# Optimization experiments

Measured on AMD Instinct MI355X. Metric: run time of the kernel, lower is better.

Reference implementation:

```python
import jax, jax.numpy as jnp
import numpy as np

B, S, H, NH, T = 4, 512, 512, 8, 3
DH = H // NH
DTS = H // T  # 170, per-timescale encoder width
EPS = 1e-5

def _ln(x, g, b):
    m = jnp.mean(x, axis=-1, keepdims=True)
    v = jnp.mean((x - m) ** 2, axis=-1, keepdims=True)
    return (x - m) * jax.lax.rsqrt(v + EPS) * g + b

def _gelu(x):
    return jax.nn.gelu(x, approximate=False)

def _mha(x, qkv_W, qkv_b, out_W, out_b, mask):
    # x: [B,S,H]; qkv_W: [H,3H]; mask: [B,S,S] float additive or None
    qkv = x @ qkv_W + qkv_b
    q, k, v = jnp.split(qkv, 3, axis=-1)
    q = q.reshape(B, S, NH, DH)
    k = k.reshape(B, S, NH, DH)
    v = v.reshape(B, S, NH, DH)
    scores = jnp.einsum('bqhd,bkhd->bhqk', q, k) / jnp.sqrt(jnp.float32(DH))
    if mask is not None:
        scores = scores + mask[:, None, :, :]
    attn = jax.nn.softmax(scores, axis=-1)
    o = jnp.einsum('bhqk,bkhd->bqhd', attn, v).reshape(B, S, H)
    return o @ out_W + out_b

def setup_inputs() -> dict:
    key = jax.random.key(0)
    ks = jax.random.split(key, 32)
    r = lambda i, shape, s=0.02: (jax.random.normal(ks[i], shape, dtype=jnp.float32) * s)
    inp = {}
    inp['x'] = jax.random.normal(ks[0], (B, S, H), dtype=jnp.float32)
    inp['timestamps'] = jax.random.uniform(ks[1], (B, S), dtype=jnp.float32) * 1e6
    # per-timescale encoders (stacked over T)
    inp['enc_W'] = r(2, (T, 2, DTS), 0.5)
    inp['enc_b'] = jnp.zeros((T, DTS), jnp.float32)
    inp['enc_ln_g'] = jnp.ones((T, DTS), jnp.float32)
    inp['enc_ln_b'] = jnp.zeros((T, DTS), jnp.float32)
    # per-timescale MHA
    inp['qkv_W'] = r(3, (T, H, 3 * H))
    inp['qkv_b'] = jnp.zeros((T, 3 * H), jnp.float32)
    inp['attn_out_W'] = r(4, (T, H, H))
    inp['attn_out_b'] = jnp.zeros((T, H), jnp.float32)
    # time mixer
    inp['mixer_W1'] = r(5, (T * H, H))
    inp['mixer_b1'] = jnp.zeros((H,), jnp.float32)
    inp['mixer_ln_g'] = jnp.ones((H,), jnp.float32)
    inp['mixer_ln_b'] = jnp.zeros((H,), jnp.float32)
    inp['mixer_W2'] = r(6, (H, T))
    inp['mixer_b2'] = jnp.zeros((T,), jnp.float32)
    # transformer encoder layer (post-norm, gelu, ffn=4H)
    inp['el_qkv_W'] = r(7, (H, 3 * H))
    inp['el_qkv_b'] = jnp.zeros((3 * H,), jnp.float32)
    inp['el_out_W'] = r(8, (H, H))
    inp['el_out_b'] = jnp.zeros((H,), jnp.float32)
    inp['el_ln1_g'] = jnp.ones((H,), jnp.float32)
    inp['el_ln1_b'] = jnp.zeros((H,), jnp.float32)
    inp['el_ff_W1'] = r(9, (H, 4 * H))
    inp['el_ff_b1'] = jnp.zeros((4 * H,), jnp.float32)
    inp['el_ff_W2'] = r(10, (4 * H, H))
    inp['el_ff_b2'] = jnp.zeros((H,), jnp.float32)
    inp['el_ln2_g'] = jnp.ones((H,), jnp.float32)
    inp['el_ln2_b'] = jnp.zeros((H,), jnp.float32)
    # output projection
    inp['op_W'] = r(11, (H, H))
    inp['op_b'] = jnp.zeros((H,), jnp.float32)
    inp['op_ln_g'] = jnp.ones((H,), jnp.float32)
    inp['op_ln_b'] = jnp.zeros((H,), jnp.float32)
    return inp

def reference(x, timestamps, enc_W, enc_b, enc_ln_g, enc_ln_b, qkv_W, qkv_b, attn_out_W, attn_out_b,
              mixer_W1, mixer_b1, mixer_ln_g, mixer_ln_b, mixer_W2, mixer_b2,
              el_qkv_W, el_qkv_b, el_out_W, el_out_b, el_ln1_g, el_ln1_b,
              el_ff_W1, el_ff_b1, el_ff_W2, el_ff_b2, el_ln2_g, el_ln2_b,
              op_W, op_b, op_ln_g, op_ln_b):
    # pairwise time features [B,S,S]
    time_diff = timestamps[:, :, None] - timestamps[:, None, :]
    direction = jnp.sign(time_diff)
    magnitude = jnp.log1p(jnp.abs(time_diff) / 3600.0)
    outs = []
    for i in range(T):
        mag = magnitude / (10.0 ** i)
        tf = jnp.stack([direction, mag], axis=-1)            # [B,S,S,2]
        e = tf @ enc_W[i] + enc_b[i]                          # [B,S,S,DTS]
        e = _gelu(_ln(e, enc_ln_g[i], enc_ln_b[i]))
        mask = jnp.mean(e, axis=-1)                           # [B,S,S] additive attn mask
        outs.append(_mha(x, qkv_W[i], qkv_b[i], attn_out_W[i], attn_out_b[i], mask))
    combined = jnp.concatenate(outs, axis=-1)                 # [B,S,T*H]
    m = _gelu(_ln(combined @ mixer_W1 + mixer_b1, mixer_ln_g, mixer_ln_b))
    mix = jax.nn.softmax(m @ mixer_W2 + mixer_b2, axis=-1)    # [B,S,T]
    weighted = sum(mix[..., i:i + 1] * outs[i] for i in range(T))
    # post-norm transformer encoder layer
    sa = _mha(weighted, el_qkv_W, el_qkv_b, el_out_W, el_out_b, None)
    h1 = _ln(weighted + sa, el_ln1_g, el_ln1_b)
    ff = _gelu(h1 @ el_ff_W1 + el_ff_b1) @ el_ff_W2 + el_ff_b2
    h2 = _ln(h1 + ff, el_ln2_g, el_ln2_b)
    out = _ln(h2 @ op_W + op_b, op_ln_g, op_ln_b)
    return out
```

## Files before the change

### kernel.cpp

```cpp
#include <hip/hip_runtime.h>
#include <hip/hip_bf16.h>
#include <math.h>

#define Bq 4
#define Sq 512
#define Hq 512
#define NHq 8
#define Tq 3
#define DTSq 170
#define BSq 2048
#define NLUT 2048
#define MAGMAXf 5.6304994f

typedef float f32x4 __attribute__((ext_vector_type(4)));
typedef __bf16 bf16x4 __attribute__((ext_vector_type(4)));
typedef __bf16 bf16x8 __attribute__((ext_vector_type(8)));

__device__ __forceinline__ float gelu_f(float x){
  return 0.5f * x * (1.0f + erff(x * 0.70710678118654752f));
}

__device__ __forceinline__ void gload16(const void* g, void* l){
  __builtin_amdgcn_global_load_lds((const __attribute__((address_space(1))) void*)g,
                                   (__attribute__((address_space(3))) void*)l, 16, 0, 0);
}

__device__ __forceinline__ float waveReduceSum(float v){
  #pragma unroll
  for (int off = 32; off > 0; off >>= 1) v += __shfl_xor(v, off);
  return v;
}

__device__ __forceinline__ float blockReduce(float v, float* red){
  int tid = threadIdx.x;
  __syncthreads();
  red[tid] = v; __syncthreads();
  for (int s = 128; s > 0; s >>= 1){
    if (tid < s) red[tid] += red[tid + s];
    __syncthreads();
  }
  return red[0];
}

struct CvtEnt { const float* W; __bf16* WT; int ldw, ldt, ntn, start; };
struct CvtArgs { CvtEnt e[12]; };

__global__ __launch_bounds__(256) void prep_all(
    const float* __restrict__ x, __bf16* __restrict__ xb,
    CvtArgs a,
    const float* __restrict__ encW, const float* __restrict__ encB,
    const float* __restrict__ g, const float* __restrict__ be,
    float* __restrict__ lut)
{
  __shared__ float T[64][65];
  __shared__ float red[256];
  __shared__ float sw0[DTSq], sw1[DTSq], sbc[DTSq], sg[DTSq], sbe[DTSq];
  __shared__ float sS[6];
  int bid = blockIdx.x, tid = threadIdx.x;

  if (bid < 1024){
    int idx = (bid * 256 + tid) * 4;
    float4 v = *(const float4*)&x[idx];
    bf16x4 r; r[0]=(__bf16)v.x; r[1]=(__bf16)v.y; r[2]=(__bf16)v.z; r[3]=(__bf16)v.w;
    *(bf16x4*)&xb[idx] = r;
    return;
  }
  if (bid < 1024 + 1792){
    int wb = bid - 1024;
    int i = 0;
    #pragma unroll
    for (int k = 1; k < 12; ++k) if (wb >= a.e[k].start) i = k;
    const float* W = a.e[i].W;
    __bf16* WT = a.e[i].WT;
    int ldw = a.e[i].ldw, ldt = a.e[i].ldt;
    int local = wb - a.e[i].start;
    int tn = local % a.e[i].ntn, tk = local / a.e[i].ntn;
    int n0 = tn * 64, k0 = tk * 64;
    #pragma unroll
    for (int q = 0; q < 16; ++q){
      int lin = q * 256 + tid;
      int r = lin >> 6, c = lin & 63;
      T[r][c] = W[(size_t)(k0 + r) * ldw + n0 + c];
    }
    __syncthreads();
    #pragma unroll
    for (int q = 0; q < 16; ++q){
      int lin = q * 256 + tid;
      int n = lin >> 6, k = lin & 63;
      WT[(size_t)(n0 + n) * ldt + k0 + k] = (__bf16)T[k][n];
    }
    return;
  }
  int local = bid - (1024 + 1792);
  int td = local >> 3, echunk = local & 7;
  int t = td / 3, dsel = td % 3;
  float d = (float)(dsel - 1);
  const float* W0 = encW + t * 2 * DTSq;
  const float* W1 = W0 + DTSq;
  const float* Bv = encB + t * DTSq;
  float w0 = (tid < DTSq) ? W0[tid] : 0.f;
  float w1 = (tid < DTSq) ? W1[tid] : 0.f;
  float bv = (tid < DTSq) ? Bv[tid] : 0.f;
  const float invD = 1.0f / (float)DTSq;
  float m0 = blockReduce(w0, red) * invD;
  float m1 = blockReduce(w1, red) * invD;
  float mb = blockReduce(bv, red) * invD;
  float c0 = (tid < DTSq) ? (w0 - m0) : 0.f;
  float c1 = (tid < DTSq) ? (w1 - m1) : 0.f;
  float cb = (tid < DTSq) ? (bv - mb) : 0.f;
  if (tid < DTSq){
    sw0[tid] = c0; sw1[tid] = c1; sbc[tid] = cb;
    sg[tid] = g[t * DTSq + tid]; sbe[tid] = be[t * DTSq + tid];
  }
  float pa = blockReduce(c0 * c0, red) * invD;
  float pb = blockReduce(c1 * c1, red) * invD;
  float pc = blockReduce(c0 * c1, red) * invD;
  float pd = blockReduce(c0 * cb, red) * invD;
  float pe = blockReduce(c1 * cb, red) * invD;
  float pf = blockReduce(cb * cb, red) * invD;
  if (tid == 0){ sS[0]=pa; sS[1]=pb; sS[2]=pc; sS[3]=pd; sS[4]=pe; sS[5]=pf; }
  __syncthreads();
  float A = sS[0], Bs = sS[1], Cs = sS[2], Ds = sS[3], Es = sS[4], Fs = sS[5];
  int e = echunk * 256 + tid;
  float tscale = (t == 0) ? 1.f : ((t == 1) ? 0.1f : 0.01f);
  float m = (MAGMAXf / (float)(NLUT - 1)) * (float)e * tscale;
  float var = fabsf(d) * A + m * m * Bs + Fs + 2.f * (d * m * Cs + d * Ds + m * Es);
  float rs = rsqrtf(var + 1e-5f);
  float sum = 0.f;
  for (int c = 0; c < DTSq; ++c){
    float ee = fmaf(m, sw1[c], fmaf(d, sw0[c], sbc[c]));
    float n = fmaf(ee * rs, sg[c], sbe[c]);
    sum += n * 0.5f * (1.0f + erff(n * 0.70710678118654752f));
  }
  lut[td * NLUT + e] = sum * (1.0f / (float)DTSq);
}

__global__ __launch_bounds__(256) void mask_fill(const float* __restrict__ ts,
                                                 const float* __restrict__ lut,
                                                 __bf16* __restrict__ maskbuf){
  int bi = blockIdx.x;
  int b = bi >> 9, i = bi & 511;
  float tsi = ts[bi];
  for (int j0 = 0; j0 < Sq; j0 += 256){
    int j = j0 + threadIdx.x;
    float dt = tsi - ts[(b << 9) + j];
    int dsel = (dt > 0.f) ? 2 : ((dt < 0.f) ? 0 : 1);
    float mag = log1pf(fabsf(dt) * (1.0f / 3600.0f));
    float u = mag * ((float)(NLUT - 1) / MAGMAXf);
    int i0 = (int)u; if (i0 > NLUT - 2) i0 = NLUT - 2;
    float f = u - (float)i0;
    #pragma unroll
    for (int t = 0; t < Tq; ++t){
      const float* lp = lut + (t * 3 + dsel) * NLUT + i0;
      float v = lp[0] + f * (lp[1] - lp[0]);
      maskbuf[(((size_t)(t * Bq + b) * Sq + i) * Sq) + j] = (__bf16)v;
    }
  }
}

template<int BM, int BN, int BK>
__global__ __launch_bounds__(256) void gemm_pipe(
    const __bf16* __restrict__ A, int lda, size_t sAz,
    const __bf16* __restrict__ BT, int ldb, size_t sBz,
    const float* __restrict__ bias, int sBiasz,
    float* __restrict__ C32, __bf16* __restrict__ C16, int ldc, size_t sCz,
    int K, int act)
{
  constexpr int MF = BM / 32;
  constexpr int NF = BN / 32;
  constexpr int ROWB = BK * 2;
  constexpr int SWZM = (BK == 64) ? 7 : 15;
  constexpr int ALOADS = BM * ROWB / 4096;
  constexpr int BLOADS = BN * ROWB / 4096;
  constexpr int LOADS = ALOADS + BLOADS;
  constexpr int ABYTES = BM * ROWB;
  constexpr int BBYTES = BN * ROWB;
  __shared__ __bf16 lds[(2 * (ABYTES + BBYTES)) / 2];
  int tid = threadIdx.x;

  int gx = gridDim.x, nwg = gx * gridDim.y;
  int lin = blockIdx.x + gx * blockIdx.y;
  int q8 = nwg >> 3;
  int swz = (lin & 7) * q8 + (lin >> 3);
  int bx = swz % gx, by = swz / gx;

  int z = blockIdx.z;
  A  += (size_t)z * sAz;
  BT += (size_t)z * sBz;
  const float* bz = bias ? bias + (size_t)z * sBiasz : nullptr;
  size_t cbase = (size_t)z * sCz;
  int brow = by * BM, bcol = bx * BN;

  int lane = tid & 63, w = tid >> 6;
  int wr = (w >> 1) * (BM / 2), wc = (w & 1) * (BN / 2);
  int lr = lane & 15, lg = lane >> 4;

  f32x4 acc[MF][NF];
  #pragma unroll
  for (int m = 0; m < MF; ++m)
    #pragma unroll
    for (int n = 0; n < NF; ++n) acc[m][n] = (f32x4){0.f, 0.f, 0.f, 0.f};

  char* lbase = (char*)lds;

  auto stage = [&](int buf, int ko){
    char* ab = lbase + buf * (ABYTES + BBYTES);
    #pragma unroll
    for (int qq = 0; qq < ALOADS; ++qq){
      int byte = (qq * 256 + tid) * 16;
      int row = byte / ROWB, col = byte % ROWB;
      int src = col ^ ((row & SWZM) << 4);
      gload16(&A[(size_t)(brow + row) * lda + ko + (src >> 1)], ab + byte);
    }
    char* bb = ab + ABYTES;
    #pragma unroll
    for (int qq = 0; qq < BLOADS; ++qq){
      int byte = (qq * 256 + tid) * 16;
      int row = byte / ROWB, col = byte % ROWB;
      int src = col ^ ((row & SWZM) << 4);
      gload16(&BT[(size_t)(bcol + row) * ldb + ko + (src >> 1)], bb + byte);
    }
  };

  stage(0, 0);
  int nk = K / BK;
  for (int kt = 0; kt < nk; ++kt){
    int cur = kt & 1;
    if (kt + 1 < nk){
      stage(cur ^ 1, (kt + 1) * BK);
      if constexpr (LOADS == 3)      asm volatile("s_waitcnt vmcnt(3)" ::: "memory");
      else if constexpr (LOADS == 4) asm volatile("s_waitcnt vmcnt(4)" ::: "memory");
      else                           asm volatile("s_waitcnt vmcnt(6)" ::: "memory");
    } else {
      asm volatile("s_waitcnt vmcnt(0)" ::: "memory");
    }
    __builtin_amdgcn_s_barrier();
    __builtin_amdgcn_sched_barrier(0);
    char* ab = lbase + cur * (ABYTES + BBYTES);
    char* bb = ab + ABYTES;
    #pragma unroll
    for (int s = 0; s < BK / 32; ++s){
      bf16x8 af[MF], bfr[NF];
      #pragma unroll
      for (int m = 0; m < MF; ++m){
        int row = wr + m * 16 + lr;
        int col = (s * 64 + lg * 16) ^ ((row & SWZM) << 4);
        af[m] = *(const bf16x8*)(ab + row * ROWB + col);
      }
      #pragma unroll
      for (int n = 0; n < NF; ++n){
        int row = wc + n * 16 + lr;
        int col = (s * 64 + lg * 16) ^ ((row & SWZM) << 4);
        bfr[n] = *(const bf16x8*)(bb + row * ROWB + col);
      }
      #pragma unroll
      for (int m = 0; m < MF; ++m)
        #pragma unroll
        for (int n = 0; n < NF; ++n)
          acc[m][n] = __builtin_amdgcn_mfma_f32_16x16x32_bf16(af[m], bfr[n], acc[m][n], 0, 0, 0);
    }
    asm volatile("" ::: "memory");
    __builtin_amdgcn_s_barrier();
  }

  #pragma unroll
  for (int m = 0; m < MF; ++m){
    #pragma unroll
    for (int n = 0; n < NF; ++n){
      int col = bcol + wc + n * 16 + lr;
      float bv = bz ? bz[col] : 0.f;
      #pragma unroll
      for (int j = 0; j < 4; ++j){
        int row = brow + wr + m * 16 + lg * 4 + j;
        float v = acc[m][n][j] + bv;
        if (act) v = gelu_f(v);
        size_t idx = cbase + (size_t)row * ldc + col;
        if (C32) C32[idx] = v;
        if (C16) C16[idx] = (__bf16)v;
      }
    }
  }
}

template<bool HM>
__global__ __launch_bounds__(256) void flash_attn(
    const __bf16* __restrict__ qkv, size_t sQz,
    const __bf16* __restrict__ vt,  size_t sVz,
    const __bf16* __restrict__ mask, size_t sMz,
    __bf16* __restrict__ ctx, size_t sCz)
{
  int t = blockIdx.z;
  qkv += (size_t)t * sQz;
  vt  += (size_t)t * sVz;
  ctx += (size_t)t * sCz;
  const __bf16* mk = HM ? mask + (size_t)t * sMz : nullptr;

  int lin = blockIdx.x + (blockIdx.y << 3);
  int swz = (lin & 7) * 32 + (lin >> 3);
  int io = (swz & 7) * 64;
  int bh = swz >> 3;
  int b = bh >> 3, h = bh & 7;

  constexpr int TB = 8192;
  constexpr int BUFB = HM ? 3 * TB : 2 * TB;
  __shared__ char lds[2 * BUFB + (HM ? 0 : TB)];
  char* lb = lds;
  int tid = threadIdx.x, lane = tid & 63, w = tid >> 6;
  int lr = lane & 15, lg = lane >> 4;

  const __bf16* qrow = &qkv[(size_t)(b * Sq + io + w * 16 + lr) * 1536 + h * 64];
  bf16x8 q0 = *(const bf16x8*)&qrow[lg * 8];
  bf16x8 q1 = *(const bf16x8*)&qrow[32 + lg * 8];

  auto stage = [&](int buf, int jo){
    char* kb = lb + buf * BUFB;
    #pragma unroll
    for (int qq = 0; qq < 2; ++qq){
      int byte = (qq * 256 + tid) * 16;
      int row = byte >> 7;
      int src = (byte & 127) ^ ((row & 7) << 4);
      gload16(&qkv[(size_t)(b * Sq + jo + row) * 1536 + 512 + h * 64 + (src >> 1)], kb + byte);
    }
    char* vb = kb + TB;
    #pragma unroll
    for (int qq = 0; qq < 2; ++qq){
      int byte = (qq * 256 + tid) * 16;
      int row = byte >> 7;
      int src = (byte & 127) ^ ((row & 7) << 4);
      gload16(&vt[((size_t)bh * 64 + row) * Sq + jo + (src >> 1)], vb + byte);
    }
    if constexpr (HM){
      char* mb = vb + TB;
      #pragma unroll
      for (int qq = 0; qq < 2; ++qq){
        int byte = (qq * 256 + tid) * 16;
        int row = byte >> 7;
        int src = (byte & 127) ^ ((row & 7) << 4);
        gload16(&mk[(size_t)(b * Sq + io + row) * Sq + jo + (src >> 1)], mb + byte);
      }
    }
  };

  f32x4 o[4];
  #pragma unroll
  for (int n = 0; n < 4; ++n) o[n] = (f32x4){0.f, 0.f, 0.f, 0.f};
  float mrow[4] = {-1e30f, -1e30f, -1e30f, -1e30f};
  float lrow[4] = {0.f, 0.f, 0.f, 0.f};

  stage(0, 0);
  #pragma unroll
  for (int kt = 0; kt < 8; ++kt){
    int cur = kt & 1;

    if (kt + 1 < 8){
      stage(cur ^ 1, (kt + 1) << 6);
      if constexpr (HM) asm volatile("s_waitcnt vmcnt(6)" ::: "memory");
      else              asm volatile("s_waitcnt vmcnt(4)" ::: "memory");
    } else {
      asm volatile("s_waitcnt vmcnt(0)" ::: "memory");
    }
    __builtin_amdgcn_s_barrier();
    __builtin_amdgcn_sched_barrier(0);

    char* kb = lb + cur * BUFB;
    char* vb = kb + TB;
    char* mb = HM ? vb + TB : lb + 2 * BUFB;

    f32x4 s4[4];
    #pragma unroll
    for (int n = 0; n < 4; ++n) s4[n] = (f32x4){0.f, 0.f, 0.f, 0.f};
    __builtin_amdgcn_s_setprio(1);
    #pragma unroll
    for (int s = 0; s < 2; ++s){
      bf16x8 aq = s ? q1 : q0;
      #pragma unroll
      for (int n = 0; n < 4; ++n){
        int row = n * 16 + lr;
        int colb = (s * 64 + lg * 16) ^ ((row & 7) << 4);
        bf16x8 bk = *(const bf16x8*)(kb + row * 128 + colb);
        s4[n] = __builtin_amdgcn_mfma_f32_16x16x32_bf16(aq, bk, s4[n], 0, 0, 0);
      }
    }
    __builtin_amdgcn_s_setprio(0);

    float sv[4][4];
    #pragma unroll
    for (int n = 0; n < 4; ++n){
      #pragma unroll
      for (int reg = 0; reg < 4; ++reg){
        float v = s4[n][reg] * 0.125f;
        if constexpr (HM){
          int row = w * 16 + lg * 4 + reg;
          int off = ((n * 16 + lr) * 2) ^ ((row & 7) << 4);
          v += (float)*(const __bf16*)(mb + row * 128 + off);
        }
        sv[n][reg] = v;
      }
    }

    #pragma unroll
    for (int reg = 0; reg < 4; ++reg){
      float pmax = fmaxf(fmaxf(sv[0][reg], sv[1][reg]), fmaxf(sv[2][reg], sv[3][reg]));
      #pragma unroll
      for (int off = 1; off < 16; off <<= 1) pmax = fmaxf(pmax, __shfl_xor(pmax, off));
      if (pmax > mrow[reg] + 8.0f){
        float corr = __expf(mrow[reg] - pmax);
        mrow[reg] = pmax;
        lrow[reg] *= corr;
        #pragma unroll
        for (int n = 0; n < 4; ++n) o[n][reg] *= corr;
      }
      float rs = 0.f;
      #pragma unroll
      for (int n = 0; n < 4; ++n){
        float p = __expf(sv[n][reg] - mrow[reg]);
        sv[n][reg] = p;
        rs += p;
      }
      #pragma unroll
      for (int off = 1; off < 16; off <<= 1) rs += __shfl_xor(rs, off);
      lrow[reg] += rs;
    }

    #pragma unroll
    for (int n = 0; n < 4; ++n)
      #pragma unroll
      for (int reg = 0; reg < 4; ++reg){
        int row = w * 16 + lg * 4 + reg;
        int off = ((n * 16 + lr) * 2) ^ ((row & 7) << 4);
        *(__bf16*)(mb + row * 128 + off) = (__bf16)sv[n][reg];
      }
    __builtin_amdgcn_s_setprio(1);
    #pragma unroll
    for (int s = 0; s < 2; ++s){
      int arow = w * 16 + lr;
      int acol = (s * 64 + lg * 16) ^ ((arow & 7) << 4);
      bf16x8 ap = *(const bf16x8*)(mb + arow * 128 + acol);
      #pragma unroll
      for (int n = 0; n < 4; ++n){
        int row = n * 16 + lr;
        int colb = (s * 64 + lg * 16) ^ ((row & 7) << 4);
        bf16x8 bv = *(const bf16x8*)(vb + row * 128 + colb);
        o[n] = __builtin_amdgcn_mfma_f32_16x16x32_bf16(ap, bv, o[n], 0, 0, 0);
      }
    }
    __builtin_amdgcn_s_setprio(0);

    asm volatile("" ::: "memory");
    __builtin_amdgcn_s_barrier();
  }

  #pragma unroll
  for (int reg = 0; reg < 4; ++reg){
    float inv = 1.0f / lrow[reg];
    int row = b * Sq + io + w * 16 + lg * 4 + reg;
    #pragma unroll
    for (int n = 0; n < 4; ++n)
      ctx[(size_t)row * Hq + h * 64 + n * 16 + lr] = (__bf16)(o[n][reg] * inv);
  }
}

__global__ __launch_bounds__(256) void ln_rows(const float* __restrict__ in,
                                               const float* __restrict__ res,
                                               const float* __restrict__ g,
                                               const float* __restrict__ bb,
                                               float* __restrict__ out32,
                                               __bf16* __restrict__ out16,
                                               int do_gelu){
  int row = blockIdx.x * 4 + (threadIdx.x >> 6);
  int lane = threadIdx.x & 63;
  const float* ir = in + (size_t)row * Hq;
  const float* rr = res ? res + (size_t)row * Hq : nullptr;
  float x[8]; float s = 0.f, sq = 0.f;
  #pragma unroll
  for (int k = 0; k < 8; ++k){
    int c = lane + 64 * k;
    float v = ir[c];
    if (rr) v += rr[c];
    x[k] = v; s += v; sq += v * v;
  }
  s = waveReduceSum(s); sq = waveReduceSum(sq);
  float mean = s * (1.0f / Hq);
  float var = fmaxf(sq * (1.0f / Hq) - mean * mean, 0.f);
  float rstd = rsqrtf(var + 1e-5f);
  #pragma unroll
  for (int k = 0; k < 8; ++k){
    int c = lane + 64 * k;
    float y = (x[k] - mean) * rstd * g[c] + bb[c];
    if (do_gelu) y = gelu_f(y);
    if (out32) out32[(size_t)row * Hq + c] = y;
    if (out16) out16[(size_t)row * Hq + c] = (__bf16)y;
  }
}

__global__ __launch_bounds__(256) void ln_mixer_weighted(const float* __restrict__ in,
                                                         const float* __restrict__ g,
                                                         const float* __restrict__ bb,
                                                         const float* __restrict__ W2,
                                                         const float* __restrict__ b2,
                                                         const __bf16* __restrict__ comb,
                                                         float* __restrict__ out32,
                                                         __bf16* __restrict__ out16){
  int row = blockIdx.x * 4 + (threadIdx.x >> 6);
  int lane = threadIdx.x & 63;
  const float* ir = in + (size_t)row * Hq;
  float x[8]; float s = 0.f, sq = 0.f;
  #pragma unroll
  for (int k = 0; k < 8; ++k){
    int c = lane + 64 * k;
    float v = ir[c];
    x[k] = v; s += v; sq += v * v;
  }
  s = waveReduceSum(s); sq = waveReduceSum(sq);
  float mean = s * (1.0f / Hq);
  float var = fmaxf(sq * (1.0f / Hq) - mean * mean, 0.f);
  float rstd = rsqrtf(var + 1e-5f);
  float a0 = 0.f, a1 = 0.f, a2 = 0.f;
  #pragma unroll
  for (int k = 0; k < 8; ++k){
    int c = lane + 64 * k;
    float y = gelu_f((x[k] - mean) * rstd * g[c] + bb[c]);
    const float* wv = W2 + c * 3;
    a0 = fmaf(y, wv[0], a0); a1 = fmaf(y, wv[1], a1); a2 = fmaf(y, wv[2], a2);
  }
  a0 = waveReduceSum(a0) + b2[0];
  a1 = waveReduceSum(a1) + b2[1];
  a2 = waveReduceSum(a2) + b2[2];
  float mx = fmaxf(a0, fmaxf(a1, a2));
  float e0 = __expf(a0 - mx), e1 = __expf(a1 - mx), e2 = __expf(a2 - mx);
  float inv = 1.0f / (e0 + e1 + e2);
  float m0 = e0 * inv, m1 = e1 * inv, m2 = e2 * inv;
  const __bf16* cr = comb + (size_t)row * 1536;
  #pragma unroll
  for (int k = 0; k < 8; ++k){
    int c = lane + 64 * k;
    float v = m0 * (float)cr[c] + m1 * (float)cr[512 + c] + m2 * (float)cr[1024 + c];
    out32[(size_t)row * Hq + c] = v;
    out16[(size_t)row * Hq + c] = (__bf16)v;
  }
}

__global__ __launch_bounds__(256) void transpose_v(const __bf16* __restrict__ qkv, size_t sQz,
                                                   __bf16* __restrict__ vt, size_t sVz){
  int t = blockIdx.z;
  qkv += (size_t)t * sQz;
  vt  += (size_t)t * sVz;
  int bh = blockIdx.y, b = bh >> 3, h = bh & 7;
  int so = blockIdx.x * 64;
  __shared__ __bf16 T[64][72];
  int tid = threadIdx.x;
  #pragma unroll
  for (int q = 0; q < 16; ++q){
    int lin = q * 256 + tid;
    int r = lin >> 6, c = lin & 63;
    T[r][c] = qkv[(size_t)(b * Sq + so + r) * 1536 + 1024 + h * 64 + c];
  }
  __syncthreads();
  #pragma unroll
  for (int q = 0; q < 16; ++q){
    int lin = q * 256 + tid;
    int d = lin >> 6, s = lin & 63;
    vt[((size_t)bh * 64 + d) * Sq + so + s] = T[s][d];
  }
}

extern "C" void kernel_launch(void* const* d_in, const int* in_sizes, int n_in,
                              void* d_out, int out_size, void* d_ws, size_t ws_size,
                              hipStream_t stream){
  const float* x         = (const float*)d_in[0];
  const float* ts        = (const float*)d_in[1];
  const float* enc_W     = (const float*)d_in[2];
  const float* enc_b     = (const float*)d_in[3];
  const float* enc_ln_g  = (const float*)d_in[4];
  const float* enc_ln_b  = (const float*)d_in[5];
  const float* qkv_W     = (const float*)d_in[6];
  const float* qkv_b     = (const float*)d_in[7];
  const float* aout_W    = (const float*)d_in[8];
  const float* aout_b    = (const float*)d_in[9];
  const float* mx_W1     = (const float*)d_in[10];
  const float* mx_b1     = (const float*)d_in[11];
  const float* mx_ln_g   = (const float*)d_in[12];
  const float* mx_ln_b   = (const float*)d_in[13];
  const float* mx_W2     = (const float*)d_in[14];
  const float* mx_b2     = (const float*)d_in[15];
  const float* el_qkv_W  = (const float*)d_in[16];
  const float* el_qkv_b  = (const float*)d_in[17];
  const float* el_out_W  = (const float*)d_in[18];
  const float* el_out_b  = (const float*)d_in[19];
  const float* el_ln1_g  = (const float*)d_in[20];
  const float* el_ln1_b  = (const float*)d_in[21];
  const float* el_ff_W1  = (const float*)d_in[22];
  const float* el_ff_b1  = (const float*)d_in[23];
  const float* el_ff_W2  = (const float*)d_in[24];
  const float* el_ff_b2  = (const float*)d_in[25];
  const float* el_ln2_g  = (const float*)d_in[26];
  const float* el_ln2_b  = (const float*)d_in[27];
  const float* op_W      = (const float*)d_in[28];
  const float* op_b      = (const float*)d_in[29];
  const float* op_ln_g   = (const float*)d_in[30];
  const float* op_ln_b   = (const float*)d_in[31];

  float* ws = (float*)d_ws;
  size_t o = 0;
  __bf16* MASKBb = (__bf16*)(ws + o); o += 1572864;
  __bf16* XB     = (__bf16*)(ws + o); o += 524288;
  __bf16* qkvT   = (__bf16*)(ws + o); o += 1179648;
  __bf16* aoutT  = (__bf16*)(ws + o); o += 393216;
  __bf16* mx1T   = (__bf16*)(ws + o); o += 393216;
  __bf16* elqkvT = (__bf16*)(ws + o); o += 393216;
  __bf16* eloutT = (__bf16*)(ws + o); o += 131072;
  __bf16* ff1T   = (__bf16*)(ws + o); o += 524288;
  __bf16* ff2T   = (__bf16*)(ws + o); o += 524288;
  __bf16* opT    = (__bf16*)(ws + o); o += 131072;
  __bf16* QKVb   = (__bf16*)(ws + o); o += 4718592;
  __bf16* VTb    = (__bf16*)(ws + o); o += 1572864;
  __bf16* FFBb   = (__bf16*)(ws + o); o += 2097152;
  __bf16* CTXb   = (__bf16*)(ws + o); o += 1572864;
  __bf16* COMBb  = (__bf16*)(ws + o); o += 1572864;
  float*  MBUF   = ws + o;            o += 1048576;
  float*  WEI    = ws + o;            o += 1048576;
  __bf16* WEIb   = (__bf16*)(ws + o); o += 524288;
  float*  SA     = ws + o;            o += 1048576;
  float*  H1     = ws + o;            o += 1048576;
  __bf16* H1b    = (__bf16*)(ws + o); o += 524288;
  float*  H2     = ws + o;            o += 1048576;
  __bf16* H2b    = (__bf16*)(ws + o); o += 524288;
  float*  LUTB   = ws + o;            o += 9 * NLUT;
  float*  OPO    = MBUF;

  {
    CvtArgs ca;
    for (int t = 0; t < 3; ++t)
      ca.e[t] = {qkv_W + (size_t)t * 512 * 1536, qkvT + (size_t)t * 1536 * 512, 1536, 512, 24, 192 * t};
    for (int t = 0; t < 3; ++t)
      ca.e[3 + t] = {aout_W + (size_t)t * 512 * 512, aoutT + (size_t)t * 512 * 512, 512, 512, 8, 576 + 64 * t};
    ca.e[6]  = {mx_W1,    mx1T,   512,  1536, 8,  768};
    ca.e[7]  = {el_qkv_W, elqkvT, 1536, 512,  24, 960};
    ca.e[8]  = {el_out_W, eloutT, 512,  512,  8,  1152};
    ca.e[9]  = {el_ff_W1, ff1T,   2048, 512,  32, 1216};
    ca.e[10] = {el_ff_W2, ff2T,   512,  2048, 8,  1472};
    ca.e[11] = {op_W,     opT,    512,  512,  8,  1728};
    prep_all<<<1024 + 1792 + 72, 256, 0, stream>>>(x, XB, ca, enc_W, enc_b,
                                                   enc_ln_g, enc_ln_b, LUTB);
  }
  mask_fill<<<BSq, 256, 0, stream>>>(ts, LUTB, MASKBb);

  gemm_pipe<128,64,64><<<dim3(24, 16, 3), 256, 0, stream>>>(XB, 512, 0, qkvT, 512, (size_t)1536 * 512,
      qkv_b, 1536, nullptr, QKVb, 1536, (size_t)2048 * 1536, 512, 0);
  transpose_v<<<dim3(8, 32, 3), 256, 0, stream>>>(QKVb, (size_t)2048 * 1536, VTb, (size_t)32 * 64 * 512);
  flash_attn<true><<<dim3(8, 32, 3), 256, 0, stream>>>(QKVb, (size_t)2048 * 1536,
      VTb, (size_t)32 * 64 * 512, MASKBb, (size_t)4 * 512 * 512, CTXb, (size_t)2048 * 512);
  gemm_pipe<64,32,128><<<dim3(16, 32, 3), 256, 0, stream>>>(CTXb, 512, (size_t)2048 * 512, aoutT, 512, (size_t)512 * 512,
      aout_b, 512, nullptr, COMBb, 1536, 512, 512, 0);

  gemm_pipe<64,32,128><<<dim3(16, 32, 1), 256, 0, stream>>>(COMBb, 1536, 0, mx1T, 1536, 0,
      mx_b1, 0, MBUF, nullptr, 512, 0, 1536, 0);
  ln_mixer_weighted<<<512, 256, 0, stream>>>(MBUF, mx_ln_g, mx_ln_b, mx_W2, mx_b2, COMBb, WEI, WEIb);

  gemm_pipe<128,64,64><<<dim3(24, 16, 1), 256, 0, stream>>>(WEIb, 512, 0, elqkvT, 512, 0,
      el_qkv_b, 0, nullptr, QKVb, 1536, 0, 512, 0);
  transpose_v<<<dim3(8, 32, 1), 256, 0, stream>>>(QKVb, 0, VTb, 0);
  flash_attn<false><<<dim3(8, 32, 1), 256, 0, stream>>>(QKVb, 0, VTb, 0, nullptr, 0, CTXb, 0);
  gemm_pipe<64,32,128><<<dim3(16, 32, 1), 256, 0, stream>>>(CTXb, 512, 0, eloutT, 512, 0,
      el_out_b, 0, SA, nullptr, 512, 0, 512, 0);
  ln_rows<<<512, 256, 0, stream>>>(WEI, SA, el_ln1_g, el_ln1_b, H1, H1b, 0);
  gemm_pipe<128,64,64><<<dim3(32, 16, 1), 256, 0, stream>>>(H1b, 512, 0, ff1T, 512, 0,
      el_ff_b1, 0, nullptr, FFBb, 2048, 0, 512, 1);
  gemm_pipe<64,32,128><<<dim3(16, 32, 1), 256, 0, stream>>>(FFBb, 2048, 0, ff2T, 2048, 0,
      el_ff_b2, 0, SA, nullptr, 512, 0, 2048, 0);
  ln_rows<<<512, 256, 0, stream>>>(H1, SA, el_ln2_g, el_ln2_b, H2, H2b, 0);

  gemm_pipe<64,32,128><<<dim3(16, 32, 1), 256, 0, stream>>>(H2b, 512, 0, opT, 512, 0,
      op_b, 0, OPO, nullptr, 512, 0, 512, 0);
  ln_rows<<<512, 256, 0, stream>>>(OPO, nullptr, op_ln_g, op_ln_b, (float*)d_out, nullptr, 0);
}
```

Before: 208.7 us.

## Compute timestamp mask inside flash attention from LDS-resident LUT

Removes the mask_fill kernel and the bf16 [3,B,S,S] mask buffer. The masked flash attention now loads timestamps and a smaller per-timescale LUT into LDS and computes the additive mask per score element (log1p plus interpolation). The LUT shrinks from 2048 to 512 entries so it fits in LDS, which cuts LUT prep blocks but coarsens interpolation accuracy. This trades mask memory traffic and a kernel launch for extra ALU work per score inside attention.

```diff
diff --git a/kernel.cpp b/kernel.cpp
--- a/kernel.cpp
+++ b/kernel.cpp
@@ -9,7 +9,7 @@
 #define Tq 3
 #define DTSq 170
 #define BSq 2048
-#define NLUT 2048
+#define NLUT 512
 #define MAGMAXf 5.6304994f
 
 typedef float f32x4 __attribute__((ext_vector_type(4)));
@@ -92,7 +92,7 @@
     return;
   }
   int local = bid - (1024 + 1792);
-  int td = local >> 3, echunk = local & 7;
+  int td = local >> 1, echunk = local & 1;
   int t = td / 3, dsel = td % 3;
   float d = (float)(dsel - 1);
   const float* W0 = encW + t * 2 * DTSq;
@@ -135,29 +135,6 @@
   lut[td * NLUT + e] = sum * (1.0f / (float)DTSq);
 }
 
-__global__ __launch_bounds__(256) void mask_fill(const float* __restrict__ ts,
-                                                 const float* __restrict__ lut,
-                                                 __bf16* __restrict__ maskbuf){
-  int bi = blockIdx.x;
-  int b = bi >> 9, i = bi & 511;
-  float tsi = ts[bi];
-  for (int j0 = 0; j0 < Sq; j0 += 256){
-    int j = j0 + threadIdx.x;
-    float dt = tsi - ts[(b << 9) + j];
-    int dsel = (dt > 0.f) ? 2 : ((dt < 0.f) ? 0 : 1);
-    float mag = log1pf(fabsf(dt) * (1.0f / 3600.0f));
-    float u = mag * ((float)(NLUT - 1) / MAGMAXf);
-    int i0 = (int)u; if (i0 > NLUT - 2) i0 = NLUT - 2;
-    float f = u - (float)i0;
-    #pragma unroll
-    for (int t = 0; t < Tq; ++t){
-      const float* lp = lut + (t * 3 + dsel) * NLUT + i0;
-      float v = lp[0] + f * (lp[1] - lp[0]);
-      maskbuf[(((size_t)(t * Bq + b) * Sq + i) * Sq) + j] = (__bf16)v;
-    }
-  }
-}
-
 template<int BM, int BN, int BK>
 __global__ __launch_bounds__(256) void gemm_pipe(
     const __bf16* __restrict__ A, int lda, size_t sAz,
@@ -286,14 +263,14 @@
 __global__ __launch_bounds__(256) void flash_attn(
     const __bf16* __restrict__ qkv, size_t sQz,
     const __bf16* __restrict__ vt,  size_t sVz,
-    const __bf16* __restrict__ mask, size_t sMz,
+    const float* __restrict__ tsg,
+    const float* __restrict__ lutg,
     __bf16* __restrict__ ctx, size_t sCz)
 {
   int t = blockIdx.z;
   qkv += (size_t)t * sQz;
   vt  += (size_t)t * sVz;
   ctx += (size_t)t * sCz;
-  const __bf16* mk = HM ? mask + (size_t)t * sMz : nullptr;
 
   int lin = blockIdx.x + (blockIdx.y << 3);
   int swz = (lin & 7) * 32 + (lin >> 3);
@@ -302,15 +279,29 @@
   int b = bh >> 3, h = bh & 7;
 
   constexpr int TB = 8192;
-  constexpr int BUFB = HM ? 3 * TB : 2 * TB;
-  __shared__ char lds[2 * BUFB + (HM ? 0 : TB)];
+  constexpr int BUFB = 2 * TB;
+  __shared__ char lds[2 * BUFB + TB + (HM ? 8192 : 0)];
   char* lb = lds;
+  char* psb = lb + 2 * BUFB;
+  float* tsL  = (float*)(lb + 2 * BUFB + TB);
+  float* lutL = (float*)(lb + 2 * BUFB + TB + 2048);
   int tid = threadIdx.x, lane = tid & 63, w = tid >> 6;
   int lr = lane & 15, lg = lane >> 4;
 
   const __bf16* qrow = &qkv[(size_t)(b * Sq + io + w * 16 + lr) * 1536 + h * 64];
   bf16x8 q0 = *(const bf16x8*)&qrow[lg * 8];
   bf16x8 q1 = *(const bf16x8*)&qrow[32 + lg * 8];
+
+  if constexpr (HM){
+    const float* tsrow = tsg + b * Sq;
+    const float* lrow  = lutg + t * 3 * NLUT;
+    #pragma unroll
+    for (int qq = 0; qq < 2; ++qq){
+      int c = qq * 256 + tid;
+      if (c < 128) gload16(tsrow + c * 4, (char*)tsL + c * 16);
+      else         gload16(lrow + (c - 128) * 4, (char*)lutL + (c - 128) * 16);
+    }
+  }
 
   auto stage = [&](int buf, int jo){
     char* kb = lb + buf * BUFB;
@@ -329,16 +320,6 @@
       int src = (byte & 127) ^ ((row & 7) << 4);
       gload16(&vt[((size_t)bh * 64 + row) * Sq + jo + (src >> 1)], vb + byte);
     }
-    if constexpr (HM){
-      char* mb = vb + TB;
-      #pragma unroll
-      for (int qq = 0; qq < 2; ++qq){
-        int byte = (qq * 256 + tid) * 16;
-        int row = byte >> 7;
-        int src = (byte & 127) ^ ((row & 7) << 4);
-        gload16(&mk[(size_t)(b * Sq + io + row) * Sq + jo + (src >> 1)], mb + byte);
-      }
-    }
   };
 
   f32x4 o[4];
@@ -351,11 +332,11 @@
   #pragma unroll
   for (int kt = 0; kt < 8; ++kt){
     int cur = kt & 1;
+    int jo = kt << 6;
 
     if (kt + 1 < 8){
       stage(cur ^ 1, (kt + 1) << 6);
-      if constexpr (HM) asm volatile("s_waitcnt vmcnt(6)" ::: "memory");
-      else              asm volatile("s_waitcnt vmcnt(4)" ::: "memory");
+      asm volatile("s_waitcnt vmcnt(4)" ::: "memory");
     } else {
       asm volatile("s_waitcnt vmcnt(0)" ::: "memory");
     }
@@ -364,7 +345,6 @@
 
     char* kb = lb + cur * BUFB;
     char* vb = kb + TB;
-    char* mb = HM ? vb + TB : lb + 2 * BUFB;
 
     f32x4 s4[4];
     #pragma unroll
@@ -384,18 +364,33 @@
     __builtin_amdgcn_s_setprio(0);
 
     float sv[4][4];
-    #pragma unroll
-    for (int n = 0; n < 4; ++n){
-      #pragma unroll
-      for (int reg = 0; reg < 4; ++reg){
-        float v = s4[n][reg] * 0.125f;
-        if constexpr (HM){
-          int row = w * 16 + lg * 4 + reg;
-          int off = ((n * 16 + lr) * 2) ^ ((row & 7) << 4);
-          v += (float)*(const __bf16*)(mb + row * 128 + off);
+    if constexpr (HM){
+      float tsj[4], tsi[4];
+      #pragma unroll
+      for (int n = 0; n < 4; ++n) tsj[n] = tsL[jo + n * 16 + lr];
+      #pragma unroll
+      for (int reg = 0; reg < 4; ++reg) tsi[reg] = tsL[io + w * 16 + lg * 4 + reg];
+      #pragma unroll
+      for (int n = 0; n < 4; ++n){
+        #pragma unroll
+        for (int reg = 0; reg < 4; ++reg){
+          float dt = tsi[reg] - tsj[n];
+          int dsel = (dt > 0.f) ? 2 : ((dt < 0.f) ? 0 : 1);
+          float mag = log1pf(fabsf(dt) * (1.0f / 3600.0f));
+          float u = mag * ((float)(NLUT - 1) / MAGMAXf);
+          int i0 = (int)u; if (i0 > NLUT - 2) i0 = NLUT - 2;
+          float f = u - (float)i0;
+          const float* lp = lutL + dsel * NLUT + i0;
+          float mv = lp[0] + f * (lp[1] - lp[0]);
+          sv[n][reg] = s4[n][reg] * 0.125f + mv;
         }
-        sv[n][reg] = v;
-      }
+      }
+    } else {
+      #pragma unroll
+      for (int n = 0; n < 4; ++n)
+        #pragma unroll
+        for (int reg = 0; reg < 4; ++reg)
+          sv[n][reg] = s4[n][reg] * 0.125f;
     }
 
     #pragma unroll
@@ -428,14 +423,14 @@
       for (int reg = 0; reg < 4; ++reg){
         int row = w * 16 + lg * 4 + reg;
         int off = ((n * 16 + lr) * 2) ^ ((row & 7) << 4);
-        *(__bf16*)(mb + row * 128 + off) = (__bf16)sv[n][reg];
+        *(__bf16*)(psb + row * 128 + off) = (__bf16)sv[n][reg];
       }
     __builtin_amdgcn_s_setprio(1);
     #pragma unroll
     for (int s = 0; s < 2; ++s){
       int arow = w * 16 + lr;
       int acol = (s * 64 + lg * 16) ^ ((arow & 7) << 4);
-      bf16x8 ap = *(const bf16x8*)(mb + arow * 128 + acol);
+      bf16x8 ap = *(const bf16x8*)(psb + arow * 128 + acol);
       #pragma unroll
       for (int n = 0; n < 4; ++n){
         int row = n * 16 + lr;
@@ -602,7 +597,7 @@
 
   float* ws = (float*)d_ws;
   size_t o = 0;
-  __bf16* MASKBb = (__bf16*)(ws + o); o += 1572864;
+  float*  LUTB   = ws + o;            o += 9 * NLUT;
   __bf16* XB     = (__bf16*)(ws + o); o += 524288;
   __bf16* qkvT   = (__bf16*)(ws + o); o += 1179648;
   __bf16* aoutT  = (__bf16*)(ws + o); o += 393216;
@@ -625,7 +620,6 @@
   __bf16* H1b    = (__bf16*)(ws + o); o += 524288;
   float*  H2     = ws + o;            o += 1048576;
   __bf16* H2b    = (__bf16*)(ws + o); o += 524288;
-  float*  LUTB   = ws + o;            o += 9 * NLUT;
   float*  OPO    = MBUF;
 
   {
@@ -640,16 +634,15 @@
     ca.e[9]  = {el_ff_W1, ff1T,   2048, 512,  32, 1216};
     ca.e[10] = {el_ff_W2, ff2T,   512,  2048, 8,  1472};
     ca.e[11] = {op_W,     opT,    512,  512,  8,  1728};
-    prep_all<<<1024 + 1792 + 72, 256, 0, stream>>>(x, XB, ca, enc_W, enc_b,
+    prep_all<<<1024 + 1792 + 18, 256, 0, stream>>>(x, XB, ca, enc_W, enc_b,
                                                    enc_ln_g, enc_ln_b, LUTB);
   }
-  mask_fill<<<BSq, 256, 0, stream>>>(ts, LUTB, MASKBb);
 
   gemm_pipe<128,64,64><<<dim3(24, 16, 3), 256, 0, stream>>>(XB, 512, 0, qkvT, 512, (size_t)1536 * 512,
       qkv_b, 1536, nullptr, QKVb, 1536, (size_t)2048 * 1536, 512, 0);
   transpose_v<<<dim3(8, 32, 3), 256, 0, stream>>>(QKVb, (size_t)2048 * 1536, VTb, (size_t)32 * 64 * 512);
   flash_attn<true><<<dim3(8, 32, 3), 256, 0, stream>>>(QKVb, (size_t)2048 * 1536,
-      VTb, (size_t)32 * 64 * 512, MASKBb, (size_t)4 * 512 * 512, CTXb, (size_t)2048 * 512);
+      VTb, (size_t)32 * 64 * 512, ts, LUTB, CTXb, (size_t)2048 * 512);
   gemm_pipe<64,32,128><<<dim3(16, 32, 3), 256, 0, stream>>>(CTXb, 512, (size_t)2048 * 512, aoutT, 512, (size_t)512 * 512,
       aout_b, 512, nullptr, COMBb, 1536, 512, 512, 0);
 
@@ -660,7 +653,7 @@
   gemm_pipe<128,64,64><<<dim3(24, 16, 1), 256, 0, stream>>>(WEIb, 512, 0, elqkvT, 512, 0,
       el_qkv_b, 0, nullptr, QKVb, 1536, 0, 512, 0);
   transpose_v<<<dim3(8, 32, 1), 256, 0, stream>>>(QKVb, 0, VTb, 0);
-  flash_attn<false><<<dim3(8, 32, 1), 256, 0, stream>>>(QKVb, 0, VTb, 0, nullptr, 0, CTXb, 0);
+  flash_attn<false><<<dim3(8, 32, 1), 256, 0, stream>>>(QKVb, 0, VTb, 0, nullptr, nullptr, CTXb, 0);
   gemm_pipe<64,32,128><<<dim3(16, 32, 1), 256, 0, stream>>>(CTXb, 512, 0, eloutT, 512, 0,
       el_out_b, 0, SA, nullptr, 512, 0, 512, 0);
   ln_rows<<<512, 256, 0, stream>>>(WEI, SA, el_ln1_g, el_ln1_b, H1, H1b, 0);
```

Result: slower. 277.5 us (+33.0%).
